# Performance work log

Hardware: AMD Instinct MI355X
Metric: run time of the kernel (lower is better)

The kernel has to match this reference:

```python
import jax, jax.numpy as jnp
import numpy as np

HEADS = 4
DIM_HEAD = 32
SCALE = DIM_HEAD ** -0.5


def setup_inputs() -> dict:
    key = jax.random.key(0)
    k1, k2, k3 = jax.random.split(key, 3)
    dim, hidden = 256, HEADS * DIM_HEAD
    x = jax.random.normal(k1, (4, dim, 64, 64), dtype=jnp.float32)
    w_qkv = jax.random.normal(k2, (hidden * 3, dim), dtype=jnp.float32) * (dim ** -0.5)
    w_out = jax.random.normal(k3, (dim, hidden), dtype=jnp.float32) * (hidden ** -0.5)
    b_out = jnp.zeros((dim,), dtype=jnp.float32)
    return {"x": x, "w_qkv": w_qkv, "w_out": w_out, "b_out": b_out}


def reference(x, w_qkv, w_out, b_out):
    b, c, h, w = x.shape
    # 1x1 conv (no bias) == channel matmul
    qkv = jnp.einsum('bchw,oc->bohw', x, w_qkv)           # [b, 3*hidden, h, w]
    q, k, v = jnp.split(qkv, 3, axis=1)
    def to_heads(t):
        # [b, heads*d, h, w] -> [b, heads, h*w, d]
        return t.reshape(b, HEADS, DIM_HEAD, h * w).transpose(0, 1, 3, 2)
    q, k, v = to_heads(q) * SCALE, to_heads(k), to_heads(v)
    sim = jnp.einsum('bhid,bhjd->bhij', q, k)             # [b, heads, hw, hw]
    attn = jax.nn.softmax(sim, axis=-1)
    out = jnp.einsum('bhij,bhjd->bhid', attn, v)          # [b, heads, hw, d]
    out = out.transpose(0, 1, 3, 2).reshape(b, HEADS * DIM_HEAD, h, w)
    # output 1x1 conv with bias
    return jnp.einsum('bchw,oc->bohw', out, w_out) + b_out[None, :, None, None]
```

## Files before the change

kernel.cpp:

```cpp
#include <hip/hip_runtime.h>
#include <hip/hip_fp16.h>

#define HEADS 4
#define DH    32
#define HW    4096
#define CIN   256
#define HID   128

using half8   = __attribute__((ext_vector_type(8))) _Float16;
using half4   = __attribute__((ext_vector_type(4))) _Float16;
using half2v  = __attribute__((ext_vector_type(2))) _Float16;
using floatx4 = __attribute__((ext_vector_type(4))) float;

#define SHIFT2 4.328085122666891f
#define WQSCALE 0.25508275947f

static __device__ __forceinline__ half2v pk2(float a, float b) {
  return __builtin_bit_cast(half2v, __builtin_amdgcn_cvt_pkrtz(a, b));
}

__global__ __launch_bounds__(256) void qkv_fused(
    const float* __restrict__ w, const float* __restrict__ x,
    _Float16* __restrict__ Qw, _Float16* __restrict__ Kw,
    _Float16* __restrict__ Vtw)
{
  __shared__ float t[64][65];
  __shared__ _Float16 As[64][72];
  __shared__ _Float16 Bs[64][72];
  const int mt = blockIdx.x, nt = blockIdx.y;
  const int b = nt >> 6, p0 = (nt & 63) * 64;
  const int tid = threadIdx.x;
  const int wv = tid >> 6, lane = tid & 63, lm = lane & 15, quad = lane >> 4;
  const float wscale = (mt < 2) ? WQSCALE : 1.0f;

  const float* Ag = w + (size_t)(mt * 64) * CIN;
  const float* xb = x + (size_t)b * CIN * HW + p0;

  floatx4 acc[4] = {{0,0,0,0},{0,0,0,0},{0,0,0,0},{0,0,0,0}};

  for (int kq = 0; kq < 4; ++kq) {
    __syncthreads();
    #pragma unroll
    for (int i = 0; i < 4; ++i) {
      int ci = tid + i * 256;
      int cc = ci >> 4, p4 = (ci & 15) * 4;
      *(float4*)&t[cc][p4] =
          *(const float4*)(xb + (size_t)(kq * 64 + cc) * HW + p4);
    }
    #pragma unroll
    for (int i = 0; i < 2; ++i) {
      int ci = tid + i * 256;
      int r = ci >> 3, c8 = (ci & 7) * 8;
      const float* src = Ag + (size_t)r * CIN + kq * 64 + c8;
      float4 u0 = *(const float4*)(src);
      float4 u1 = *(const float4*)(src + 4);
      half8 h = {(_Float16)(u0.x * wscale), (_Float16)(u0.y * wscale),
                 (_Float16)(u0.z * wscale), (_Float16)(u0.w * wscale),
                 (_Float16)(u1.x * wscale), (_Float16)(u1.y * wscale),
                 (_Float16)(u1.z * wscale), (_Float16)(u1.w * wscale)};
      *(half8*)&As[r][c8] = h;
    }
    __syncthreads();
    #pragma unroll
    for (int i = 0; i < 2; ++i) {
      int idx = tid + i * 256;
      int p = idx >> 3, c0 = (idx & 7) * 8;
      half8 v;
      #pragma unroll
      for (int k = 0; k < 8; ++k) v[k] = (_Float16)t[c0 + k][p];
      *(half8*)&Bs[p][c0] = v;
    }
    __syncthreads();
    #pragma unroll
    for (int ks = 0; ks < 2; ++ks) {
      half8 a = *(const half8*)&As[wv * 16 + lm][ks * 32 + quad * 8];
      #pragma unroll
      for (int ns = 0; ns < 4; ++ns) {
        half8 bf = *(const half8*)&Bs[ns * 16 + lm][ks * 32 + quad * 8];
        acc[ns] = __builtin_amdgcn_mfma_f32_16x16x32_f16(a, bf, acc[ns], 0, 0, 0);
      }
    }
  }

  const int sec = mt >> 1;
  const int o_base = (mt & 1) * 64 + wv * 16 + quad * 4;
  const int hh = o_base >> 5, dd = o_base & 31;
  const int bh = b * HEADS + hh;
  if (sec < 2) {
    _Float16* dst = (sec == 0) ? Qw : Kw;
    #pragma unroll
    for (int ns = 0; ns < 4; ++ns) {
      int p = p0 + ns * 16 + lm;
      half4 v = {(_Float16)acc[ns][0], (_Float16)acc[ns][1],
                 (_Float16)acc[ns][2], (_Float16)acc[ns][3]};
      *(half4*)(dst + ((size_t)bh * HW + p) * DH + dd) = v;
    }
  } else {
    #pragma unroll
    for (int ns = 0; ns < 4; ++ns) {
      int p = p0 + ns * 16 + lm;
      #pragma unroll
      for (int r = 0; r < 4; ++r)
        Vtw[((size_t)bh * DH + dd + r) * HW + p] = (_Float16)acc[ns][r];
    }
  }
}

__global__ __launch_bounds__(256) void attn(
    const _Float16* __restrict__ Qw, const _Float16* __restrict__ Kw,
    const _Float16* __restrict__ Vtw, _Float16* __restrict__ Ot)
{
  __shared__ _Float16 ks[2][2][64][40];
  __shared__ _Float16 vt[2][2][32][74];

  const int bh = blockIdx.y, qt = blockIdx.x;
  const int tid = threadIdx.x;
  const int wv = tid >> 6, lane = tid & 63, lm = lane & 15, quad = lane >> 4;

  const _Float16* qbase =
      Qw + ((size_t)bh * HW + qt * 128 + wv * 16 + lm) * DH + quad * 8;
  const half8 qa0 = *(const half8*)qbase;
  const half8 qa1 = *(const half8*)(qbase + (size_t)64 * DH);

  const _Float16 one = (_Float16)1.0f;
  const half4 ones4 = {one, one, one, one};
  const floatx4 shiftc = {-SHIFT2, -SHIFT2, -SHIFT2, -SHIFT2};

  floatx4 oT[2][2] = {{{0,0,0,0},{0,0,0,0}},{{0,0,0,0},{0,0,0,0}}};
  floatx4 l4[2]    = {{0,0,0,0},{0,0,0,0}};

  const _Float16* kbase = Kw  + (size_t)bh * HW * DH;
  const _Float16* vbase = Vtw + (size_t)bh * DH * HW;
  const int kr = tid >> 2, kc = (tid & 3) * 8;
  const int vr = tid >> 3, vc = (tid & 7) * 8;

  half8 kA = *(const half8*)(kbase + (size_t)kr * DH + kc);
  half8 vA = *(const half8*)(vbase + (size_t)vr * HW + vc);
  half8 kB = *(const half8*)(kbase + ((size_t)64 + kr) * DH + kc);
  half8 vB = *(const half8*)(vbase + (size_t)vr * HW + 64 + vc);
  *(half8*)&ks[0][0][kr][kc] = kA;
  *(half8*)&vt[0][0][vr][vc] = vA;
  *(half8*)&ks[0][1][kr][kc] = kB;
  *(half8*)&vt[0][1][vr][vc] = vB;
  kA = *(const half8*)(kbase + ((size_t)128 + kr) * DH + kc);
  vA = *(const half8*)(vbase + (size_t)vr * HW + 128 + vc);
  kB = *(const half8*)(kbase + ((size_t)192 + kr) * DH + kc);
  vB = *(const half8*)(vbase + (size_t)vr * HW + 192 + vc);
  __syncthreads();

  for (int it = 0; it < HW / 128; ++it) {
    const int ph = it & 1, nx = ph ^ 1;
    *(half8*)&ks[nx][0][kr][kc] = kA;
    *(half8*)&vt[nx][0][vr][vc] = vA;
    *(half8*)&ks[nx][1][kr][kc] = kB;
    *(half8*)&vt[nx][1][vr][vc] = vB;
    size_t koff = (size_t)(it * 2 + 4) * 64;
    if (koff > HW - 128) koff = HW - 128;
    kA = *(const half8*)(kbase + (koff + kr) * DH + kc);
    vA = *(const half8*)(vbase + (size_t)vr * HW + koff + vc);
    kB = *(const half8*)(kbase + (koff + 64 + kr) * DH + kc);
    vB = *(const half8*)(vbase + (size_t)vr * HW + koff + 64 + vc);

    #pragma unroll
    for (int sub = 0; sub < 2; ++sub) {
      #pragma unroll
      for (int f = 0; f < 4; ++f) {
        half8 kb = *(const half8*)&ks[ph][sub][f * 16 + lm][quad * 8];
        floatx4 sT0 = __builtin_amdgcn_mfma_f32_16x16x32_f16(kb, qa0, shiftc, 0, 0, 0);
        floatx4 sT1 = __builtin_amdgcn_mfma_f32_16x16x32_f16(kb, qa1, shiftc, 0, 0, 0);
        half2v a0 = pk2(__builtin_amdgcn_exp2f(sT0[0]), __builtin_amdgcn_exp2f(sT0[1]));
        half2v b0 = pk2(__builtin_amdgcn_exp2f(sT0[2]), __builtin_amdgcn_exp2f(sT0[3]));
        half2v a1 = pk2(__builtin_amdgcn_exp2f(sT1[0]), __builtin_amdgcn_exp2f(sT1[1]));
        half2v b1 = pk2(__builtin_amdgcn_exp2f(sT1[2]), __builtin_amdgcn_exp2f(sT1[3]));
        half4 pb0 = {a0.x, a0.y, b0.x, b0.y};
        half4 pb1 = {a1.x, a1.y, b1.x, b1.y};
        l4[0] = __builtin_amdgcn_mfma_f32_16x16x16f16(ones4, pb0, l4[0], 0, 0, 0);
        l4[1] = __builtin_amdgcn_mfma_f32_16x16x16f16(ones4, pb1, l4[1], 0, 0, 0);
        #pragma unroll
        for (int g = 0; g < 2; ++g) {
          half4 va = *(const half4*)&vt[ph][sub][g * 16 + lm][f * 16 + quad * 4];
          oT[0][g] = __builtin_amdgcn_mfma_f32_16x16x16f16(va, pb0, oT[0][g], 0, 0, 0);
          oT[1][g] = __builtin_amdgcn_mfma_f32_16x16x16f16(va, pb1, oT[1][g], 0, 0, 0);
        }
      }
    }
    __syncthreads();
  }

  const int b = bh >> 2, hh = bh & 3;
  #pragma unroll
  for (int t = 0; t < 2; ++t) {
    const float inv = 1.0f / l4[t][0];
    _Float16* obase = Ot +
        ((size_t)(b * HW + qt * 128 + t * 64 + wv * 16 + lm)) * HID + hh * DH;
    #pragma unroll
    for (int g = 0; g < 2; ++g) {
      half4 v = {(_Float16)(oT[t][g][0] * inv), (_Float16)(oT[t][g][1] * inv),
                 (_Float16)(oT[t][g][2] * inv), (_Float16)(oT[t][g][3] * inv)};
      *(half4*)(obase + g * 16 + quad * 4) = v;
    }
  }
}

__global__ __launch_bounds__(256) void out_gemm(
    const float* __restrict__ wo, const _Float16* __restrict__ Ot,
    const float* __restrict__ bo, float* __restrict__ out)
{
  __shared__ _Float16 As[64][136];
  __shared__ _Float16 Bs[64][136];
  __shared__ float os[64][68];
  const int mt = blockIdx.x, nt = blockIdx.y;
  const int b = nt >> 6, p0 = (nt & 63) * 64;
  const int tid = threadIdx.x;
  const int wv = tid >> 6, lane = tid & 63, lm = lane & 15, quad = lane >> 4;

  const float* Ag = wo + (size_t)(mt * 64) * HID;
  const _Float16* B = Ot + ((size_t)b * HW + p0) * HID;

  #pragma unroll
  for (int i = 0; i < 4; ++i) {
    int ci = tid + i * 256;
    int r = ci >> 4, c8 = (ci & 15) * 8;
    const float* src = Ag + (size_t)r * HID + c8;
    float4 u0 = *(const float4*)(src);
    float4 u1 = *(const float4*)(src + 4);
    half8 h = {(_Float16)u0.x, (_Float16)u0.y, (_Float16)u0.z, (_Float16)u0.w,
               (_Float16)u1.x, (_Float16)u1.y, (_Float16)u1.z, (_Float16)u1.w};
    *(half8*)&As[r][c8] = h;
    *(half8*)&Bs[r][c8] = *(const half8*)(B + (size_t)r * HID + c8);
  }
  __syncthreads();

  floatx4 acc[4] = {{0,0,0,0},{0,0,0,0},{0,0,0,0},{0,0,0,0}};
  #pragma unroll
  for (int ks = 0; ks < 4; ++ks) {
    half8 a = *(const half8*)&As[wv * 16 + lm][ks * 32 + quad * 8];
    #pragma unroll
    for (int ns = 0; ns < 4; ++ns) {
      half8 bf = *(const half8*)&Bs[ns * 16 + lm][ks * 32 + quad * 8];
      acc[ns] = __builtin_amdgcn_mfma_f32_16x16x32_f16(a, bf, acc[ns], 0, 0, 0);
    }
  }

  #pragma unroll
  for (int ns = 0; ns < 4; ++ns)
    #pragma unroll
    for (int r = 0; r < 4; ++r)
      os[wv * 16 + quad * 4 + r][ns * 16 + lm] = acc[ns][r];
  __syncthreads();

  const int o = tid >> 2, pq = (tid & 3) * 16;
  const float bias = bo[mt * 64 + o];
  float* dst = out + ((size_t)(b * CIN + mt * 64 + o)) * HW + p0 + pq;
  #pragma unroll
  for (int j = 0; j < 4; ++j) {
    float4 v = *(const float4*)&os[o][pq + j * 4];
    v.x += bias; v.y += bias; v.z += bias; v.w += bias;
    *(float4*)(dst + j * 4) = v;
  }
}

extern "C" void kernel_launch(void* const* d_in, const int* in_sizes, int n_in,
                              void* d_out, int out_size, void* d_ws, size_t ws_size,
                              hipStream_t stream)
{
  const float* x     = (const float*)d_in[0];
  const float* w_qkv = (const float*)d_in[1];
  const float* w_out = (const float*)d_in[2];
  const float* b_out = (const float*)d_in[3];
  float* out = (float*)d_out;

  char* ws = (char*)d_ws;
  _Float16* Ot  = (_Float16*)(ws);
  _Float16* Qw  = (_Float16*)(ws + (8u  << 20));
  _Float16* Kw  = (_Float16*)(ws + (12u << 20));
  _Float16* Vtw = (_Float16*)(ws + (16u << 20));

  dim3 blk(256);
  qkv_fused<<<dim3(6, 256), blk, 0, stream>>>(w_qkv, x, Qw, Kw, Vtw);
  attn<<<dim3(32, 16), blk, 0, stream>>>(Qw, Kw, Vtw, Ot);
  out_gemm<<<dim3(4, 256), blk, 0, stream>>>(w_out, Ot, b_out, out);
}
```

Before: 165.0 us.

## Split QKV projection into fp16 transpose pass and register-prefetched GEMM

Adds a conv_x kernel that converts x to fp16 in a pixel-major [b,hw,c] layout once. The QKV GEMM then reads that buffer directly instead of redoing the fp32 transpose for each of the 6 output tiles. The GEMM tile grows to 128 pixels with K=128 per stage, and register prefetch of the second half overlaps global loads with the first half's MFMAs. The attention grid is also flattened so consecutive blocks cover different heads. This costs an extra kernel launch plus a 8MB fp16 write and read, and the larger tiles use more shared memory, which may lower occupancy.

```diff
diff --git a/kernel.cpp b/kernel.cpp
--- a/kernel.cpp
+++ b/kernel.cpp
@@ -19,67 +19,107 @@
   return __builtin_bit_cast(half2v, __builtin_amdgcn_cvt_pkrtz(a, b));
 }
 
-__global__ __launch_bounds__(256) void qkv_fused(
-    const float* __restrict__ w, const float* __restrict__ x,
+__global__ __launch_bounds__(256) void conv_x(
+    const float* __restrict__ x, _Float16* __restrict__ Xh)
+{
+  __shared__ float t[64][65];
+  const int b = blockIdx.z, ct = blockIdx.y, pt = blockIdx.x;
+  const int tid = threadIdx.x;
+  const float* src = x + ((size_t)(b * CIN + ct * 64)) * HW + pt * 64;
+  #pragma unroll
+  for (int i = 0; i < 16; ++i) {
+    int idx = tid + i * 256;
+    int c = idx >> 6, p = idx & 63;
+    t[c][p] = src[(size_t)c * HW + p];
+  }
+  __syncthreads();
+  #pragma unroll
+  for (int pass = 0; pass < 2; ++pass) {
+    int p = (tid >> 3) + pass * 32;
+    int c0 = (tid & 7) * 8;
+    half8 v;
+    #pragma unroll
+    for (int j = 0; j < 8; ++j) v[j] = (_Float16)t[c0 + j][p];
+    *(half8*)(Xh + ((size_t)(b * HW + pt * 64 + p)) * CIN + ct * 64 + c0) = v;
+  }
+}
+
+__global__ __launch_bounds__(256) void qkv_gemm(
+    const float* __restrict__ w, const _Float16* __restrict__ Xh,
     _Float16* __restrict__ Qw, _Float16* __restrict__ Kw,
     _Float16* __restrict__ Vtw)
 {
-  __shared__ float t[64][65];
-  __shared__ _Float16 As[64][72];
-  __shared__ _Float16 Bs[64][72];
+  __shared__ _Float16 As[64][136];
+  __shared__ _Float16 Bs[128][136];
   const int mt = blockIdx.x, nt = blockIdx.y;
-  const int b = nt >> 6, p0 = (nt & 63) * 64;
+  const int b = nt >> 5, p0 = (nt & 31) * 128;
   const int tid = threadIdx.x;
   const int wv = tid >> 6, lane = tid & 63, lm = lane & 15, quad = lane >> 4;
   const float wscale = (mt < 2) ? WQSCALE : 1.0f;
 
   const float* Ag = w + (size_t)(mt * 64) * CIN;
-  const float* xb = x + (size_t)b * CIN * HW + p0;
-
-  floatx4 acc[4] = {{0,0,0,0},{0,0,0,0},{0,0,0,0},{0,0,0,0}};
-
-  for (int kq = 0; kq < 4; ++kq) {
-    __syncthreads();
+  const _Float16* Bg = Xh + ((size_t)b * HW + p0) * CIN;
+
+  float4 apre[4][2];
+  half8  bpre[8];
+  #pragma unroll
+  for (int i = 0; i < 4; ++i) {
+    int ci = tid + i * 256, r = ci >> 4, c8 = (ci & 15) * 8;
+    const float* s = Ag + (size_t)r * CIN + c8;
+    apre[i][0] = *(const float4*)s;
+    apre[i][1] = *(const float4*)(s + 4);
+  }
+  #pragma unroll
+  for (int i = 0; i < 8; ++i) {
+    int ci = tid + i * 256, r = ci >> 4, c8 = (ci & 15) * 8;
+    bpre[i] = *(const half8*)(Bg + (size_t)r * CIN + c8);
+  }
+
+  floatx4 acc[8] = {{0,0,0,0},{0,0,0,0},{0,0,0,0},{0,0,0,0},
+                    {0,0,0,0},{0,0,0,0},{0,0,0,0},{0,0,0,0}};
+
+  #pragma unroll
+  for (int kh = 0; kh < 2; ++kh) {
     #pragma unroll
     for (int i = 0; i < 4; ++i) {
-      int ci = tid + i * 256;
-      int cc = ci >> 4, p4 = (ci & 15) * 4;
-      *(float4*)&t[cc][p4] =
-          *(const float4*)(xb + (size_t)(kq * 64 + cc) * HW + p4);
-    }
-    #pragma unroll
-    for (int i = 0; i < 2; ++i) {
-      int ci = tid + i * 256;
-      int r = ci >> 3, c8 = (ci & 7) * 8;
-      const float* src = Ag + (size_t)r * CIN + kq * 64 + c8;
-      float4 u0 = *(const float4*)(src);
-      float4 u1 = *(const float4*)(src + 4);
+      int ci = tid + i * 256, r = ci >> 4, c8 = (ci & 15) * 8;
+      float4 u0 = apre[i][0], u1 = apre[i][1];
       half8 h = {(_Float16)(u0.x * wscale), (_Float16)(u0.y * wscale),
                  (_Float16)(u0.z * wscale), (_Float16)(u0.w * wscale),
                  (_Float16)(u1.x * wscale), (_Float16)(u1.y * wscale),
                  (_Float16)(u1.z * wscale), (_Float16)(u1.w * wscale)};
       *(half8*)&As[r][c8] = h;
     }
+    #pragma unroll
+    for (int i = 0; i < 8; ++i) {
+      int ci = tid + i * 256, r = ci >> 4, c8 = (ci & 15) * 8;
+      *(half8*)&Bs[r][c8] = bpre[i];
+    }
+    if (kh == 0) {
+      #pragma unroll
+      for (int i = 0; i < 4; ++i) {
+        int ci = tid + i * 256, r = ci >> 4, c8 = (ci & 15) * 8;
+        const float* s = Ag + (size_t)r * CIN + 128 + c8;
+        apre[i][0] = *(const float4*)s;
+        apre[i][1] = *(const float4*)(s + 4);
+      }
+      #pragma unroll
+      for (int i = 0; i < 8; ++i) {
+        int ci = tid + i * 256, r = ci >> 4, c8 = (ci & 15) * 8;
+        bpre[i] = *(const half8*)(Bg + (size_t)r * CIN + 128 + c8);
+      }
+    }
     __syncthreads();
     #pragma unroll
-    for (int i = 0; i < 2; ++i) {
-      int idx = tid + i * 256;
-      int p = idx >> 3, c0 = (idx & 7) * 8;
-      half8 v;
-      #pragma unroll
-      for (int k = 0; k < 8; ++k) v[k] = (_Float16)t[c0 + k][p];
-      *(half8*)&Bs[p][c0] = v;
-    }
-    __syncthreads();
-    #pragma unroll
-    for (int ks = 0; ks < 2; ++ks) {
+    for (int ks = 0; ks < 4; ++ks) {
       half8 a = *(const half8*)&As[wv * 16 + lm][ks * 32 + quad * 8];
       #pragma unroll
-      for (int ns = 0; ns < 4; ++ns) {
+      for (int ns = 0; ns < 8; ++ns) {
         half8 bf = *(const half8*)&Bs[ns * 16 + lm][ks * 32 + quad * 8];
         acc[ns] = __builtin_amdgcn_mfma_f32_16x16x32_f16(a, bf, acc[ns], 0, 0, 0);
       }
     }
+    if (kh == 0) __syncthreads();
   }
 
   const int sec = mt >> 1;
@@ -89,7 +129,7 @@
   if (sec < 2) {
     _Float16* dst = (sec == 0) ? Qw : Kw;
     #pragma unroll
-    for (int ns = 0; ns < 4; ++ns) {
+    for (int ns = 0; ns < 8; ++ns) {
       int p = p0 + ns * 16 + lm;
       half4 v = {(_Float16)acc[ns][0], (_Float16)acc[ns][1],
                  (_Float16)acc[ns][2], (_Float16)acc[ns][3]};
@@ -97,7 +137,7 @@
     }
   } else {
     #pragma unroll
-    for (int ns = 0; ns < 4; ++ns) {
+    for (int ns = 0; ns < 8; ++ns) {
       int p = p0 + ns * 16 + lm;
       #pragma unroll
       for (int r = 0; r < 4; ++r)
@@ -113,7 +153,7 @@
   __shared__ _Float16 ks[2][2][64][40];
   __shared__ _Float16 vt[2][2][32][74];
 
-  const int bh = blockIdx.y, qt = blockIdx.x;
+  const int bh = blockIdx.x & 15, qt = blockIdx.x >> 4;
   const int tid = threadIdx.x;
   const int wv = tid >> 6, lane = tid & 63, lm = lane & 15, quad = lane >> 4;
 
@@ -271,13 +311,15 @@
   float* out = (float*)d_out;
 
   char* ws = (char*)d_ws;
+  _Float16* Xh  = (_Float16*)(ws);
   _Float16* Ot  = (_Float16*)(ws);
   _Float16* Qw  = (_Float16*)(ws + (8u  << 20));
   _Float16* Kw  = (_Float16*)(ws + (12u << 20));
   _Float16* Vtw = (_Float16*)(ws + (16u << 20));
 
   dim3 blk(256);
-  qkv_fused<<<dim3(6, 256), blk, 0, stream>>>(w_qkv, x, Qw, Kw, Vtw);
-  attn<<<dim3(32, 16), blk, 0, stream>>>(Qw, Kw, Vtw, Ot);
+  conv_x<<<dim3(64, 4, 4), blk, 0, stream>>>(x, Xh);
+  qkv_gemm<<<dim3(6, 128), blk, 0, stream>>>(w_qkv, Xh, Qw, Kw, Vtw);
+  attn<<<dim3(512), blk, 0, stream>>>(Qw, Kw, Vtw, Ot);
   out_gemm<<<dim3(4, 256), blk, 0, stream>>>(w_out, Ot, b_out, out);
 }
```

Result: no change. 165.3 us (+0.2%).
